# Optimization experiments

Measured on AMD Instinct MI355X. Metric: run time of the kernel, lower is better.

The kernel has to match this reference:

```python
import jax, jax.numpy as jnp
import numpy as np

B = 2048      # env batch (graphs)
A = 8         # agents per graph (fully connected)
N = B * A     # total nodes
DIN = 192     # raw obs dim
HD = 256      # h_dim (base MLP)
MD = 256      # mem_dim (GRU)
GD = 128      # gnn_dim (per-head GATv2 out, concat=False -> head mean)
H = 4         # GAT heads
NA = 20       # n_actions
ED = 3        # edge_dim


def setup_inputs() -> dict:
    key = jax.random.key(0)
    ks = jax.random.split(key, 16)
    # fully-connected directed graph per group of A agents, no self loops
    s, d = np.meshgrid(np.arange(A), np.arange(A), indexing='ij')
    mask = s != d
    s = s[mask]; d = d[mask]                     # [A*(A-1)]
    off = (np.arange(B) * A)[:, None]
    src = (off + s[None, :]).reshape(-1)
    dst = (off + d[None, :]).reshape(-1)
    edge_index = jnp.asarray(np.stack([src, dst]), dtype=jnp.int32)  # [2, E]
    E = src.shape[0]
    p = lambda k, sh: jax.random.normal(ks[k], sh, jnp.float32) * 0.02
    return {
        'inputs': jax.random.normal(ks[0], (N, DIN), jnp.float32),
        'hidden_states': jax.random.normal(ks[1], (N, MD), jnp.float32) * 0.1,
        'edge_index': edge_index,
        'edge_attr': jax.random.uniform(ks[2], (E, ED), jnp.float32),
        # base MLP (2 layers: Linear+ReLU+LayerNorm)
        'W1': p(3, (DIN, HD)), 'b1': jnp.zeros(HD), 'g1': jnp.ones(HD), 'be1': jnp.zeros(HD),
        'W2': p(4, (HD, HD)),  'b2': jnp.zeros(HD), 'g2': jnp.ones(HD), 'be2': jnp.zeros(HD),
        # GRUCell
        'Wih': p(5, (3 * MD, HD)), 'Whh': p(6, (3 * MD, MD)),
        'bih': jnp.zeros(3 * MD), 'bhh': jnp.zeros(3 * MD),
        # GATv2Conv (edge_dim=3, heads=4, concat=False, residual)
        'Wl': p(7, (MD, H * GD)), 'bl': jnp.zeros(H * GD),
        'Wr': p(8, (MD, H * GD)), 'br': jnp.zeros(H * GD),
        'att': p(9, (H, GD)),
        'We': p(10, (ED, H * GD)),
        'Wres': p(11, (MD, GD)),
        'bg': jnp.zeros(GD),
        # head: LayerNorm + Linear
        'lng': jnp.ones(GD), 'lnb': jnp.zeros(GD),
        'Wout': p(12, (GD, NA)), 'bout': jnp.zeros(NA),
    }


def _ln(x, g, b):
    mu = jnp.mean(x, -1, keepdims=True)
    xc = x - mu
    v = jnp.mean(xc * xc, -1, keepdims=True)
    return xc * jax.lax.rsqrt(v + 1e-5) * g + b


def _fwd(inputs, hidden_states, edge_attr, edge_index,
         W1, b1, g1, be1, W2, b2, g2, be2,
         Wih, Whh, bih, bhh,
         Wl, bl, Wr, br, att, We, Wres, bg,
         lng, lnb, Wout, bout):
    src, dst = edge_index[0], edge_index[1]
    # ---- base MLP encode ----
    x = _ln(jax.nn.relu(inputs @ W1 + b1), g1, be1)
    x = _ln(jax.nn.relu(x @ W2 + b2), g2, be2)          # [N, HD]
    # ---- SimpleConv(aggr='mean', combine_root='self_loop') ----
    s = jax.ops.segment_sum(x[src], dst, num_segments=N) + x
    deg = jax.ops.segment_sum(jnp.ones(src.shape[0], x.dtype), dst, num_segments=N) + 1.0
    x = s / deg[:, None]                                 # [N, HD]
    # ---- GRUCell ----
    gi = x @ Wih.T + bih
    gh = hidden_states @ Whh.T + bhh
    ir, iz, inn = jnp.split(gi, 3, -1)
    hr, hz, hn = jnp.split(gh, 3, -1)
    r = jax.nn.sigmoid(ir + hr)
    z = jax.nn.sigmoid(iz + hz)
    n = jnp.tanh(inn + r * hn)
    h = (1.0 - z) * n + z * hidden_states                # [N, MD]
    # ---- GATv2Conv (add self loops, edge_attr fill='mean') ----
    loop = jnp.arange(N, dtype=src.dtype)
    sf = jnp.concatenate([src, loop])
    df = jnp.concatenate([dst, loop])
    ea = jnp.concatenate([edge_attr, jnp.broadcast_to(edge_attr.mean(0), (N, ED))], 0)
    xl = (h @ Wl + bl).reshape(N, H, GD)
    xr = (h @ Wr + br).reshape(N, H, GD)
    m = xl[sf] + xr[df] + (ea @ We).reshape(-1, H, GD)   # [Ef, H, GD]
    m = jnp.where(m > 0, m, 0.2 * m)                     # leaky_relu(0.2)
    logits = jnp.einsum('ehc,hc->eh', m, att)            # [Ef, H]
    mx = jax.ops.segment_max(logits, df, num_segments=N)
    ex = jnp.exp(logits - mx[df])
    den = jax.ops.segment_sum(ex, df, num_segments=N)
    alpha = ex / (den[df] + 1e-16)                       # segment softmax
    out = jax.ops.segment_sum(xl[sf] * alpha[..., None], df, num_segments=N)
    out = out.mean(1) + h @ Wres + bg                    # head mean + residual + bias
    zg = jax.nn.relu(out)                                # [N, GD]
    # ---- action head ----
    q = _ln(zg, lng, lnb) @ Wout + bout                  # [N, NA]
    return q, h


def reference(inputs, hidden_states, edge_index, edge_attr,
              W1, b1, g1, be1, W2, b2, g2, be2,
              Wih, Whh, bih, bhh,
              Wl, bl, Wr, br, att, We, Wres, bg,
              lng, lnb, Wout, bout):
    return _fwd(inputs, hidden_states, edge_attr, edge_index,
                W1, b1, g1, be1, W2, b2, g2, be2,
                Wih, Whh, bih, bhh,
                Wl, bl, Wr, br, att, We, Wres, bg,
                lng, lnb, Wout, bout)
```

## Files before the change

### kernel.cpp

```cpp
#include <hip/hip_runtime.h>
#include <hip/hip_bf16.h>

constexpr int NB  = 2048;
constexpr int AG  = 8;
constexpr int NN  = NB * AG;
constexpr int DIN = 192;
constexpr int HD  = 256;
constexpr int MD  = 256;
constexpr int GD  = 128;
constexpr int NA  = 20;
constexpr int NE  = NB * AG * (AG - 1);

typedef __attribute__((ext_vector_type(8))) short bfrag8;
typedef __attribute__((ext_vector_type(4))) short sfrag4;
typedef __attribute__((ext_vector_type(4))) float f32x4;

#define MFMA16(a, b, c) __builtin_amdgcn_mfma_f32_16x16x32_bf16((a), (b), (c), 0, 0, 0)

__device__ __forceinline__ float bf2f(__hip_bfloat16 x) { return __bfloat162float(x); }
__device__ __forceinline__ __hip_bfloat16 f2bf(float x) { return __float2bfloat16(x); }
__device__ __forceinline__ short f2bs(float x) {
    __hip_bfloat16 b = __float2bfloat16(x);
    return *reinterpret_cast<short*>(&b);
}
__device__ __forceinline__ bfrag8 ldf(const __hip_bfloat16* p) { return *(const bfrag8*)p; }
__device__ __forceinline__ bfrag8 ldf32(const float* p) {
    const f32x4 a = *(const f32x4*)p;
    const f32x4 b = *(const f32x4*)(p + 4);
    bfrag8 r;
    r[0] = f2bs(a[0]); r[1] = f2bs(a[1]); r[2] = f2bs(a[2]); r[3] = f2bs(a[3]);
    r[4] = f2bs(b[0]); r[5] = f2bs(b[1]); r[6] = f2bs(b[2]); r[7] = f2bs(b[3]);
    return r;
}
__device__ __forceinline__ float sigmf(float x) { return 1.f / (1.f + __expf(-x)); }
__device__ __forceinline__ float blo(unsigned u) { return __uint_as_float(u << 16); }
__device__ __forceinline__ float bhi(unsigned u) { return __uint_as_float(u & 0xffff0000u); }

__global__ __launch_bounds__(256) void k_prep(
    const float* __restrict__ W1, const float* __restrict__ W2,
    const float* __restrict__ Wih, const float* __restrict__ Whh,
    const float* __restrict__ Wl, const float* __restrict__ bl,
    const float* __restrict__ Wr, const float* __restrict__ br,
    const float* __restrict__ Wres, const float* __restrict__ Wout,
    const float* __restrict__ ea,
    __hip_bfloat16* __restrict__ W1T, __hip_bfloat16* __restrict__ W2T,
    __hip_bfloat16* __restrict__ WihB, __hip_bfloat16* __restrict__ WhhB,
    __hip_bfloat16* __restrict__ WcatT, float* __restrict__ WoutTf,
    float* __restrict__ bcat, float* __restrict__ ea_partials)
{
    __shared__ float sw[4][3];
    const int tid = threadIdx.x;
    if (blockIdx.x >= 3151) {
        const int b = blockIdx.x - 3151;
        float a0 = 0.f, a1 = 0.f, a2 = 0.f;
#pragma unroll
        for (int k = 0; k < 7; k++) {
            int e = b * 1792 + k * 256 + tid;
            a0 += ea[e * 3 + 0];
            a1 += ea[e * 3 + 1];
            a2 += ea[e * 3 + 2];
        }
#pragma unroll
        for (int off = 1; off < 64; off <<= 1) {
            a0 += __shfl_xor(a0, off); a1 += __shfl_xor(a1, off); a2 += __shfl_xor(a2, off);
        }
        if ((tid & 63) == 0) { sw[tid >> 6][0] = a0; sw[tid >> 6][1] = a1; sw[tid >> 6][2] = a2; }
        __syncthreads();
        if (tid == 0) {
            ea_partials[b * 3 + 0] = sw[0][0] + sw[1][0] + sw[2][0] + sw[3][0];
            ea_partials[b * 3 + 1] = sw[0][1] + sw[1][1] + sw[2][1] + sw[3][1];
            ea_partials[b * 3 + 2] = sw[0][2] + sw[1][2] + sw[2][2] + sw[3][2];
        }
        return;
    }
    int i = blockIdx.x * 256 + tid;
    if (i < 49152) { int o = i / 192, c = i % 192; W1T[i] = f2bf(W1[c * 256 + o]); return; }
    i -= 49152;
    if (i < 65536) { int o = i >> 8, c = i & 255; W2T[i] = f2bf(W2[c * 256 + o]); return; }
    i -= 65536;
    if (i < 196608) { WihB[i] = f2bf(Wih[i]); return; }
    i -= 196608;
    if (i < 196608) { WhhB[i] = f2bf(Whh[i]); return; }
    i -= 196608;
    if (i < 294912) {
        int o = i >> 8, c = i & 255;
        float v;
        if (o < 512)       v = Wl[c * 512 + o];
        else if (o < 1024) v = Wr[c * 512 + (o - 512)];
        else               v = Wres[c * 128 + (o - 1024)];
        WcatT[i] = f2bf(v); return;
    }
    i -= 294912;
    if (i < 2560) { int o = i >> 7, c = i & 127; WoutTf[i] = Wout[c * 20 + o]; return; }
    i -= 2560;
    if (i < 1152) {
        float v = 0.f;
        if (i < 512) v = bl[i]; else if (i < 1024) v = br[i - 512];
        bcat[i] = v;
    }
}

__global__ __launch_bounds__(256) void k_encode(
    const float* __restrict__ in,
    const __hip_bfloat16* __restrict__ W1T,
    const float* __restrict__ b1, const float* __restrict__ g1, const float* __restrict__ be1,
    const __hip_bfloat16* __restrict__ W2T,
    const float* __restrict__ b2, const float* __restrict__ g2, const float* __restrict__ be2,
    __hip_bfloat16* __restrict__ xm)
{
    __shared__ float sf[16][257];
    __shared__ alignas(16) __hip_bfloat16 sb[16][264];
    const int tid = threadIdx.x;
    const int lane = tid & 63, w = tid >> 6;
    const int r = lane & 15, q = lane >> 4;
    const int m0 = blockIdx.x * 16;

    {
        bfrag8 af[6];
        const float* ap = in + (size_t)(m0 + r) * DIN + q * 8;
#pragma unroll
        for (int kb = 0; kb < 6; kb++) af[kb] = ldf32(ap + kb * 32);
#pragma unroll
        for (int i = 0; i < 4; i++) {
            int t = w * 4 + i;
            const __hip_bfloat16* wp = W1T + (size_t)(t * 16 + r) * DIN + q * 8;
            bfrag8 bf[6];
#pragma unroll
            for (int kb = 0; kb < 6; kb++) bf[kb] = ldf(wp + kb * 32);
            f32x4 acc = (f32x4){0.f, 0.f, 0.f, 0.f};
#pragma unroll
            for (int kb = 0; kb < 6; kb++) acc = MFMA16(af[kb], bf[kb], acc);
            int col = t * 16 + r;
            float bias = b1[col];
#pragma unroll
            for (int reg = 0; reg < 4; reg++)
                sf[q * 4 + reg][col] = fmaxf(acc[reg] + bias, 0.f);
        }
    }
    __syncthreads();
    {
        int rowi = tid >> 4, c16 = tid & 15;
        float vals[16]; float s = 0.f, s2 = 0.f;
#pragma unroll
        for (int j = 0; j < 16; j++) { float v = sf[rowi][c16 + 16 * j]; vals[j] = v; s += v; s2 += v * v; }
#pragma unroll
        for (int off = 1; off < 16; off <<= 1) { s += __shfl_xor(s, off); s2 += __shfl_xor(s2, off); }
        float mean = s * (1.f / HD);
        float var = fmaxf(s2 * (1.f / HD) - mean * mean, 0.f);
        float rs = rsqrtf(var + 1e-5f);
#pragma unroll
        for (int j = 0; j < 16; j++) {
            int col = c16 + 16 * j;
            sb[rowi][col] = f2bf((vals[j] - mean) * rs * g1[col] + be1[col]);
        }
    }
    __syncthreads();

    {
        bfrag8 af[8];
        const __hip_bfloat16* ap = &sb[r][0];
#pragma unroll
        for (int kb = 0; kb < 8; kb++) af[kb] = ldf(ap + kb * 32 + q * 8);
        float outv[4][4];
#pragma unroll
        for (int i = 0; i < 4; i++) {
            int t = w * 4 + i;
            const __hip_bfloat16* wp = W2T + (size_t)(t * 16 + r) * HD + q * 8;
            bfrag8 bf[8];
#pragma unroll
            for (int kb = 0; kb < 8; kb++) bf[kb] = ldf(wp + kb * 32);
            f32x4 acc = (f32x4){0.f, 0.f, 0.f, 0.f};
#pragma unroll
            for (int kb = 0; kb < 8; kb++) acc = MFMA16(af[kb], bf[kb], acc);
#pragma unroll
            for (int reg = 0; reg < 4; reg++) outv[i][reg] = acc[reg];
        }
        __syncthreads();
#pragma unroll
        for (int i = 0; i < 4; i++) {
            int col = (w * 4 + i) * 16 + r;
            float bias = b2[col];
#pragma unroll
            for (int reg = 0; reg < 4; reg++)
                sf[q * 4 + reg][col] = fmaxf(outv[i][reg] + bias, 0.f);
        }
    }
    __syncthreads();
    {
        int rowi = tid >> 4, c16 = tid & 15;
        float vals[16]; float s = 0.f, s2 = 0.f;
#pragma unroll
        for (int j = 0; j < 16; j++) { float v = sf[rowi][c16 + 16 * j]; vals[j] = v; s += v; s2 += v * v; }
#pragma unroll
        for (int off = 1; off < 16; off <<= 1) { s += __shfl_xor(s, off); s2 += __shfl_xor(s2, off); }
        float mean = s * (1.f / HD);
        float var = fmaxf(s2 * (1.f / HD) - mean * mean, 0.f);
        float rs = rsqrtf(var + 1e-5f);
#pragma unroll
        for (int j = 0; j < 16; j++) {
            int col = c16 + 16 * j;
            sb[rowi][col] = f2bf((vals[j] - mean) * rs * g2[col] + be2[col]);
        }
    }
    __syncthreads();
    {
        int col = tid;
        float a0 = 0.f, a1 = 0.f;
#pragma unroll
        for (int i = 0; i < 8; i++) { a0 += bf2f(sb[i][col]); a1 += bf2f(sb[8 + i][col]); }
        xm[(size_t)(2 * blockIdx.x) * HD + col] = f2bf(a0 * 0.125f);
        xm[(size_t)(2 * blockIdx.x + 1) * HD + col] = f2bf(a1 * 0.125f);
    }
}

__global__ __launch_bounds__(256) void k_gi(
    const __hip_bfloat16* __restrict__ xm,
    const __hip_bfloat16* __restrict__ WihB,
    const float* __restrict__ bih,
    float* __restrict__ gi)
{
    const int tid = threadIdx.x;
    const int lane = tid & 63, w = tid >> 6;
    const int r = lane & 15, q = lane >> 4;
    const int m0 = (blockIdx.x >> 1) * 16;
    const int t0 = (blockIdx.x & 1) * 24;

    bfrag8 af[8];
    const __hip_bfloat16* ap = xm + (size_t)(m0 + r) * MD + q * 8;
#pragma unroll
    for (int kb = 0; kb < 8; kb++) af[kb] = ldf(ap + kb * 32);
#pragma unroll
    for (int i = 0; i < 6; i++) {
        int t = t0 + w * 6 + i;
        const __hip_bfloat16* wp = WihB + (size_t)(t * 16 + r) * MD + q * 8;
        bfrag8 bf[8];
#pragma unroll
        for (int kb = 0; kb < 8; kb++) bf[kb] = ldf(wp + kb * 32);
        f32x4 acc = (f32x4){0.f, 0.f, 0.f, 0.f};
#pragma unroll
        for (int kb = 0; kb < 8; kb++) acc = MFMA16(af[kb], bf[kb], acc);
        int col = t * 16 + r;
        float bias = bih[col];
#pragma unroll
        for (int reg = 0; reg < 4; reg++) {
            int R = m0 + q * 4 + reg;
            gi[(size_t)R * 768 + col] = acc[reg] + bias;
        }
    }
}

__global__ __launch_bounds__(256, 2) void k_gruG(
    const float* __restrict__ hprev,
    const __hip_bfloat16* __restrict__ WhhB,
    const float* __restrict__ bhh,
    const float* __restrict__ gi,
    float* __restrict__ hout)
{
    const int tid = threadIdx.x;
    const int lane = tid & 63, w = tid >> 6;
    const int r = lane & 15, q = lane >> 4;
    const int m0 = (blockIdx.x >> 2) * 128;
    const int cg = (blockIdx.x & 3) * 64;

    bfrag8 afr[2][8];
#pragma unroll
    for (int t = 0; t < 2; t++) {
        const float* ap = hprev + (size_t)(m0 + (w * 2 + t) * 16 + r) * MD + q * 8;
#pragma unroll
        for (int kb = 0; kb < 8; kb++) afr[t][kb] = ldf32(ap + kb * 32);
    }
    f32x4 acc[2][12];
#pragma unroll
    for (int t = 0; t < 2; t++)
#pragma unroll
        for (int n = 0; n < 12; n++) acc[t][n] = (f32x4){0.f, 0.f, 0.f, 0.f};

#pragma unroll
    for (int kb = 0; kb < 8; kb++) {
        bfrag8 bfB[12];
#pragma unroll
        for (int g = 0; g < 3; g++)
#pragma unroll
            for (int nj = 0; nj < 4; nj++)
                bfB[g * 4 + nj] = ldf(WhhB + (size_t)(g * 256 + cg + nj * 16 + r) * MD
                                      + kb * 32 + q * 8);
#pragma unroll
        for (int t = 0; t < 2; t++)
#pragma unroll
            for (int n = 0; n < 12; n++)
                acc[t][n] = MFMA16(bfB[n], afr[t][kb], acc[t][n]);
    }

#pragma unroll
    for (int t = 0; t < 2; t++) {
        int node = m0 + (w * 2 + t) * 16 + r;
        const float* gir = gi + (size_t)(node >> 3) * 768;
#pragma unroll
        for (int nj = 0; nj < 4; nj++) {
            int c = cg + nj * 16 + q * 4;
            f32x4 gR = *(const f32x4*)&gir[c];
            f32x4 gZ = *(const f32x4*)&gir[256 + c];
            f32x4 gN = *(const f32x4*)&gir[512 + c];
            f32x4 bR = *(const f32x4*)&bhh[c];
            f32x4 bZ = *(const f32x4*)&bhh[256 + c];
            f32x4 bN = *(const f32x4*)&bhh[512 + c];
            f32x4 hp = *(const f32x4*)&hprev[(size_t)node * MD + c];
            f32x4 hv;
#pragma unroll
            for (int reg = 0; reg < 4; reg++) {
                float rr = sigmf(gR[reg] + acc[t][0 + nj][reg] + bR[reg]);
                float zz = sigmf(gZ[reg] + acc[t][4 + nj][reg] + bZ[reg]);
                float nn = tanhf(gN[reg] + rr * (acc[t][8 + nj][reg] + bN[reg]));
                hv[reg] = (1.f - zz) * nn + zz * hp[reg];
            }
            *(f32x4*)&hout[(size_t)node * MD + c] = hv;
        }
    }
}

__global__ __launch_bounds__(256, 2) void k_xlr(
    const float* __restrict__ h,
    const __hip_bfloat16* __restrict__ WcatT,
    const float* __restrict__ bcat,
    __hip_bfloat16* __restrict__ xlr)
{
    const int tid = threadIdx.x;
    const int lane = tid & 63, w = tid >> 6;
    const int r = lane & 15, q = lane >> 4;
    const int m0 = (blockIdx.x / 9) * 128;
    const int nb = (blockIdx.x % 9) * 128;

    bfrag8 afr[2][8];
#pragma unroll
    for (int t = 0; t < 2; t++) {
        const float* ap = h + (size_t)(m0 + (w * 2 + t) * 16 + r) * MD + q * 8;
#pragma unroll
        for (int kb = 0; kb < 8; kb++) afr[t][kb] = ldf32(ap + kb * 32);
    }
    f32x4 acc[2][8];
#pragma unroll
    for (int t = 0; t < 2; t++)
#pragma unroll
        for (int n = 0; n < 8; n++) acc[t][n] = (f32x4){0.f, 0.f, 0.f, 0.f};

#pragma unroll
    for (int kb = 0; kb < 8; kb++) {
        bfrag8 bfB[8];
#pragma unroll
        for (int nj = 0; nj < 8; nj++)
            bfB[nj] = ldf(WcatT + (size_t)(nb + nj * 16 + r) * MD + kb * 32 + q * 8);
#pragma unroll
        for (int t = 0; t < 2; t++)
#pragma unroll
            for (int n = 0; n < 8; n++)
                acc[t][n] = MFMA16(bfB[n], afr[t][kb], acc[t][n]);
    }

#pragma unroll
    for (int t = 0; t < 2; t++) {
        int node = m0 + (w * 2 + t) * 16 + r;
#pragma unroll
        for (int nj = 0; nj < 8; nj++) {
            int fb = nb + nj * 16 + q * 4;
            sfrag4 pk;
#pragma unroll
            for (int reg = 0; reg < 4; reg++)
                pk[reg] = f2bs(acc[t][nj][reg] + bcat[fb + reg]);
            *(sfrag4*)&xlr[(size_t)node * 1152 + fb] = pk;
        }
    }
}

__global__ __launch_bounds__(256) void k_gat(
    const __hip_bfloat16* __restrict__ xlr,
    const float* __restrict__ ea,
    const float* __restrict__ ea_partials,
    const float* __restrict__ att,
    const float* __restrict__ We,
    const float* __restrict__ bg,
    const float* __restrict__ lng, const float* __restrict__ lnb,
    const float* __restrict__ WoutTf,
    const float* __restrict__ bout,
    float* __restrict__ qout)
{
    __shared__ alignas(16) __hip_bfloat16 sx[16][1160];
    __shared__ alignas(16) float szg[16][136];
    __shared__ float slog[2][4][8][8];
    __shared__ float smean[4];
    const int tid = threadIdx.x;
    const int lane = tid & 63, w = tid >> 6;
    const int r = lane & 15, q = lane >> 4;
    const int m0 = blockIdx.x * 16;

    if (tid < 3) {
        float s = 0.f;
        for (int i = 0; i < 64; i++) s += ea_partials[i * 3 + tid];
        smean[tid] = s * (1.f / NE);
    }
    for (int idx = tid; idx < 2304; idx += 256) {
        int row = idx / 144, off = (idx % 144) * 8;
        *(uint4*)&sx[row][off] = *(const uint4*)&xlr[(size_t)(m0 + row) * 1152 + off];
    }

    float vea[2][3];
    {
        int l = (lane < 56) ? lane : 0;
#pragma unroll
        for (int g = 0; g < 2; g++) {
            const float* ep = ea + (size_t)((blockIdx.x * 2 + g) * 56 + l) * 3;
            vea[g][0] = ep[0]; vea[g][1] = ep[1]; vea[g][2] = ep[2];
        }
    }
    __syncthreads();
    const float em0 = smean[0], em1 = smean[1], em2 = smean[2];

    {
        const int li = lane & 31, half = lane >> 5;
#pragma unroll
        for (int t = 0; t < 2; t++) {
            const int combo = w * 2 + t;
            const int gg = combo >> 2, hh = combo & 3;
            const f32x4 va  = *(const f32x4*)&att[hh * 128 + li * 4];
            const f32x4 vw0 = *(const f32x4*)&We[0 * 512 + hh * 128 + li * 4];
            const f32x4 vw1 = *(const f32x4*)&We[1 * 512 + hh * 128 + li * 4];
            const f32x4 vw2 = *(const f32x4*)&We[2 * 512 + hh * 128 + li * 4];
            float at0 = va[0],  at1 = va[1],  at2 = va[2],  at3 = va[3];
            float w00 = vw0[0], w01 = vw0[1], w02 = vw0[2], w03 = vw0[3];
            float w10 = vw1[0], w11 = vw1[1], w12 = vw1[2], w13 = vw1[3];
            float w20 = vw2[0], w21 = vw2[1], w22 = vw2[2], w23 = vw2[3];
            float ve0 = vea[gg][0], ve1 = vea[gg][1], ve2 = vea[gg][2];
            float xv[4][4];
#pragma unroll
            for (int sh2 = 0; sh2 < 4; sh2++) {
                int sL = sh2 * 2 + half;
                uint2 uxl = *(const uint2*)&sx[gg * 8 + sL][hh * 128 + li * 4];
                xv[sh2][0] = blo(uxl.x); xv[sh2][1] = bhi(uxl.x);
                xv[sh2][2] = blo(uxl.y); xv[sh2][3] = bhi(uxl.y);
            }
            float mylog = 0.f;
#pragma unroll
            for (int d = 0; d < 8; d++) {
                uint2 uxr = *(const uint2*)&sx[gg * 8 + d][512 + hh * 128 + li * 4];
                float xr0 = blo(uxr.x), xr1 = bhi(uxr.x), xr2 = blo(uxr.y), xr3 = bhi(uxr.y);
#pragma unroll
                for (int sh2 = 0; sh2 < 4; sh2++) {
                    int sL = sh2 * 2 + half;
                    int el = sL * 7 + d - (d > sL ? 1 : 0);
                    float e0 = __shfl(ve0, el), e1 = __shfl(ve1, el), e2 = __shfl(ve2, el);
                    bool slf = (sL == d);
                    e0 = slf ? em0 : e0; e1 = slf ? em1 : e1; e2 = slf ? em2 : e2;
                    float p, m;
                    m = fmaf(e2, w20, fmaf(e1, w10, fmaf(e0, w00, xv[sh2][0]))) + xr0;
                    m = fmaxf(m, 0.2f * m); p = m * at0;
                    m = fmaf(e2, w21, fmaf(e1, w11, fmaf(e0, w01, xv[sh2][1]))) + xr1;
                    m = fmaxf(m, 0.2f * m); p = fmaf(m, at1, p);
                    m = fmaf(e2, w22, fmaf(e1, w12, fmaf(e0, w02, xv[sh2][2]))) + xr2;
                    m = fmaxf(m, 0.2f * m); p = fmaf(m, at2, p);
                    m = fmaf(e2, w23, fmaf(e1, w13, fmaf(e0, w03, xv[sh2][3]))) + xr3;
                    m = fmaxf(m, 0.2f * m); p = fmaf(m, at3, p);
                    p += __shfl_xor(p, 1);  p += __shfl_xor(p, 2);  p += __shfl_xor(p, 4);
                    p += __shfl_xor(p, 8);  p += __shfl_xor(p, 16);
                    float got = __shfl(p, ((lane & 1) << 5) | li);
                    bool want = ((lane >> 3) == d) && (((lane & 7) >> 1) == sh2);
                    mylog = want ? got : mylog;
                }
            }
            ((float*)&slog[gg][hh][0][0])[lane] = mylog;
        }
    }
    __syncthreads();

    if (tid < 64) {
        int sg = tid >> 5, sh2 = (tid >> 3) & 3, d = tid & 7;
        float* L = &slog[sg][sh2][d][0];
        float mx = L[0];
#pragma unroll
        for (int s = 1; s < 8; s++) mx = fmaxf(mx, L[s]);
        float ex[8]; float den = 0.f;
#pragma unroll
        for (int s = 0; s < 8; s++) { ex[s] = __expf(L[s] - mx); den += ex[s]; }
        float inv = 1.f / (den + 1e-16f);
#pragma unroll
        for (int s = 0; s < 8; s++) L[s] = ex[s] * inv;
    }
    __syncthreads();

    {
        f32x4 acc0 = (f32x4){0.f, 0.f, 0.f, 0.f};
        f32x4 acc1 = (f32x4){0.f, 0.f, 0.f, 0.f};
        const int ggr = r >> 3, dr = r & 7;
#pragma unroll
        for (int ah = 0; ah < 4; ah++) {
            bfrag8 afA;
#pragma unroll
            for (int j = 0; j < 8; j++) {
                int k = q * 8 + j;
                float v = 0.f;
                if (k < 16) {
                    int ggk = k >> 3, s = k & 7;
                    if (ggk == ggr) v = slog[ggk][ah][dr][s];
                }
                afA[j] = f2bs(v);
            }
#pragma unroll
            for (int j2 = 0; j2 < 2; j2++) {
                int chunk = w * 2 + j2;
                bfrag8 bfB;
#pragma unroll
                for (int j = 0; j < 8; j++) {
                    int k = (q * 8 + j) & 15;
                    bfB[j] = *(const short*)&sx[k][ah * 128 + chunk * 16 + r];
                }
                if (j2 == 0) acc0 = MFMA16(afA, bfB, acc0);
                else         acc1 = MFMA16(afA, bfB, acc1);
            }
        }
#pragma unroll
        for (int j2 = 0; j2 < 2; j2++) {
            f32x4 a = j2 ? acc1 : acc0;
            int c = (w * 2 + j2) * 16 + r;
            float bgc = bg[c];
#pragma unroll
            for (int reg = 0; reg < 4; reg++) {
                int row = q * 4 + reg;
                float o = a[reg] * 0.25f + bf2f(sx[row][1024 + c]) + bgc;
                szg[row][c] = fmaxf(o, 0.f);
            }
        }
    }
    __syncthreads();

    {
        int row = tid >> 4, j = tid & 15;
        float v[8]; float s = 0.f, s2 = 0.f;
#pragma unroll
        for (int cj = 0; cj < 8; cj++) { v[cj] = szg[row][j + 16 * cj]; s += v[cj]; s2 += v[cj] * v[cj]; }
#pragma unroll
        for (int off = 1; off < 16; off <<= 1) { s += __shfl_xor(s, off); s2 += __shfl_xor(s2, off); }
        float mean = s * (1.f / GD);
        float var = fmaxf(s2 * (1.f / GD) - mean * mean, 0.f);
        float rs = rsqrtf(var + 1e-5f);
#pragma unroll
        for (int cj = 0; cj < 8; cj++) {
            int c = j + 16 * cj;
            szg[row][c] = (v[cj] - mean) * rs * lng[c] + lnb[c];
        }
    }
    __syncthreads();

    {
        int row = tid >> 4, j = tid & 15;
        for (int jj = j; jj < NA; jj += 16) {
            float a = bout[jj];
            const float* wo = WoutTf + jj * 128;
#pragma unroll
            for (int c4 = 0; c4 < 32; c4++) {
                f32x4 z = *(const f32x4*)&szg[row][c4 * 4];
                const f32x4 wv = *(const f32x4*)&wo[c4 * 4];
                a = fmaf(z[0], wv[0], a); a = fmaf(z[1], wv[1], a);
                a = fmaf(z[2], wv[2], a); a = fmaf(z[3], wv[3], a);
            }
            qout[(size_t)(m0 + row) * NA + jj] = a;
        }
    }
}

extern "C" void kernel_launch(void* const* d_in, const int* in_sizes, int n_in,
                              void* d_out, int out_size, void* d_ws, size_t ws_size,
                              hipStream_t stream) {
    const float* inp   = (const float*)d_in[0];
    const float* hid   = (const float*)d_in[1];
    const float* eatt  = (const float*)d_in[3];
    const float* W1    = (const float*)d_in[4];
    const float* b1    = (const float*)d_in[5];
    const float* g1    = (const float*)d_in[6];
    const float* be1   = (const float*)d_in[7];
    const float* W2    = (const float*)d_in[8];
    const float* b2    = (const float*)d_in[9];
    const float* g2    = (const float*)d_in[10];
    const float* be2   = (const float*)d_in[11];
    const float* Wih   = (const float*)d_in[12];
    const float* Whh   = (const float*)d_in[13];
    const float* bih   = (const float*)d_in[14];
    const float* bhh   = (const float*)d_in[15];
    const float* Wl    = (const float*)d_in[16];
    const float* bl    = (const float*)d_in[17];
    const float* Wr    = (const float*)d_in[18];
    const float* br    = (const float*)d_in[19];
    const float* att   = (const float*)d_in[20];
    const float* We    = (const float*)d_in[21];
    const float* Wres  = (const float*)d_in[22];
    const float* bg    = (const float*)d_in[23];
    const float* lng   = (const float*)d_in[24];
    const float* lnb   = (const float*)d_in[25];
    const float* Wout  = (const float*)d_in[26];
    const float* bout  = (const float*)d_in[27];

    float* qout = (float*)d_out;
    float* hout = (float*)d_out + (size_t)NN * NA;

    char* ws = (char*)d_ws;
    float*           ea_partials = (float*)ws;
    __hip_bfloat16*  xm    = (__hip_bfloat16*)(ws + 2048);
    float*           gi    = (float*)(ws + 1050624);
    __hip_bfloat16*  W1T   = (__hip_bfloat16*)(ws + 7342080);
    __hip_bfloat16*  W2T   = (__hip_bfloat16*)(ws + 7440384);
    __hip_bfloat16*  WihB  = (__hip_bfloat16*)(ws + 7571456);
    __hip_bfloat16*  WhhB  = (__hip_bfloat16*)(ws + 7964672);
    __hip_bfloat16*  WcatT = (__hip_bfloat16*)(ws + 8357888);
    float*           bcat  = (float*)(ws + 8947712);
    float*           WoutTf= (float*)(ws + 8952320);
    __hip_bfloat16*  xlr   = (__hip_bfloat16*)(ws + 8962560);

    k_prep<<<3215, 256, 0, stream>>>(W1, W2, Wih, Whh, Wl, bl, Wr, br, Wres, Wout, eatt,
                                     W1T, W2T, WihB, WhhB, WcatT, WoutTf, bcat, ea_partials);
    k_encode<<<NN / 16, 256, 0, stream>>>(inp, W1T, b1, g1, be1, W2T, b2, g2, be2, xm);
    k_gi<<<256, 256, 0, stream>>>(xm, WihB, bih, gi);
    k_gruG<<<512, 256, 0, stream>>>(hid, WhhB, bhh, gi, hout);
    k_xlr<<<1152, 256, 0, stream>>>(hout, WcatT, bcat, xlr);
    k_gat<<<NN / 16, 256, 0, stream>>>(xlr, eatt, ea_partials, att, We, bg,
                                       lng, lnb, WoutTf, bout, qout);
}
```

Baseline: 328.6 us.

## Stage xlr weight tiles in LDS via direct global-to-LDS loads and swizzle block order

The xlr GEMM kernel now uses a 2x2 wave tiling where each wave computes a 64x64 sub-tile. B weight tiles are staged into XOR-swizzled shared memory with global_load_lds, looping over four K chunks. Before, every wave loaded the full B fragments straight from global memory. Block indices in both the GRU and xlr kernels are remapped so that concurrently scheduled blocks spread across different row tiles, which may improve L2 locality across XCDs. The cost is extra __syncthreads per K step and A fragments that are now reloaded from global memory inside the K loop.

```diff
diff --git a/kernel.cpp b/kernel.cpp
--- a/kernel.cpp
+++ b/kernel.cpp
@@ -16,6 +16,10 @@
 typedef __attribute__((ext_vector_type(4))) float f32x4;
 
 #define MFMA16(a, b, c) __builtin_amdgcn_mfma_f32_16x16x32_bf16((a), (b), (c), 0, 0, 0)
+
+#define GLOAD_LDS16(g, l) __builtin_amdgcn_global_load_lds(                  \
+    (const __attribute__((address_space(1))) void*)(g),                      \
+    (__attribute__((address_space(3))) void*)(l), 16, 0, 0)
 
 __device__ __forceinline__ float bf2f(__hip_bfloat16 x) { return __bfloat162float(x); }
 __device__ __forceinline__ __hip_bfloat16 f2bf(float x) { return __float2bfloat16(x); }
@@ -259,8 +263,9 @@
     const int tid = threadIdx.x;
     const int lane = tid & 63, w = tid >> 6;
     const int r = lane & 15, q = lane >> 4;
-    const int m0 = (blockIdx.x >> 2) * 128;
-    const int cg = (blockIdx.x & 3) * 64;
+    const int bswz = (blockIdx.x & 7) * 64 + (blockIdx.x >> 3);
+    const int m0 = (bswz >> 2) * 128;
+    const int cg = (bswz & 3) * 64;
 
     bfrag8 afr[2][8];
 #pragma unroll
@@ -324,48 +329,66 @@
     const float* __restrict__ bcat,
     __hip_bfloat16* __restrict__ xlr)
 {
+    __shared__ alignas(16) __hip_bfloat16 sB[128 * 64];
     const int tid = threadIdx.x;
     const int lane = tid & 63, w = tid >> 6;
     const int r = lane & 15, q = lane >> 4;
-    const int m0 = (blockIdx.x / 9) * 128;
-    const int nb = (blockIdx.x % 9) * 128;
-
-    bfrag8 afr[2][8];
-#pragma unroll
-    for (int t = 0; t < 2; t++) {
-        const float* ap = h + (size_t)(m0 + (w * 2 + t) * 16 + r) * MD + q * 8;
-#pragma unroll
-        for (int kb = 0; kb < 8; kb++) afr[t][kb] = ldf32(ap + kb * 32);
-    }
-    f32x4 acc[2][8];
-#pragma unroll
-    for (int t = 0; t < 2; t++)
-#pragma unroll
-        for (int n = 0; n < 8; n++) acc[t][n] = (f32x4){0.f, 0.f, 0.f, 0.f};
-
-#pragma unroll
-    for (int kb = 0; kb < 8; kb++) {
-        bfrag8 bfB[8];
-#pragma unroll
-        for (int nj = 0; nj < 8; nj++)
-            bfB[nj] = ldf(WcatT + (size_t)(nb + nj * 16 + r) * MD + kb * 32 + q * 8);
-#pragma unroll
-        for (int t = 0; t < 2; t++)
-#pragma unroll
-            for (int n = 0; n < 8; n++)
-                acc[t][n] = MFMA16(bfB[n], afr[t][kb], acc[t][n]);
-    }
-
-#pragma unroll
-    for (int t = 0; t < 2; t++) {
-        int node = m0 + (w * 2 + t) * 16 + r;
-#pragma unroll
-        for (int nj = 0; nj < 8; nj++) {
-            int fb = nb + nj * 16 + q * 4;
+    const int wm = w >> 1, wn = w & 1;
+
+    const int lin = (blockIdx.x & 7) * 144 + (blockIdx.x >> 3);
+    const int m0 = (lin / 9) * 128;
+    const int nb = (lin % 9) * 128;
+
+    const int srow = tid >> 3;
+    const int sch  = (tid & 7) ^ (srow & 7);
+
+    f32x4 acc[4][4];
+#pragma unroll
+    for (int am = 0; am < 4; am++)
+#pragma unroll
+        for (int bn = 0; bn < 4; bn++) acc[am][bn] = (f32x4){0.f, 0.f, 0.f, 0.f};
+
+    for (int kt = 0; kt < 4; ++kt) {
+        if (kt) __syncthreads();
+#pragma unroll
+        for (int i = 0; i < 4; ++i) {
+            const __hip_bfloat16* gp = WcatT + (size_t)(nb + i * 32 + srow) * 256
+                                       + kt * 64 + sch * 8;
+            GLOAD_LDS16(gp, &sB[i * 2048 + tid * 8]);
+        }
+        __syncthreads();
+
+#pragma unroll
+        for (int kk = 0; kk < 2; ++kk) {
+            bfrag8 af[4], bf[4];
+#pragma unroll
+            for (int am = 0; am < 4; ++am)
+                af[am] = ldf32(h + (size_t)(m0 + wm * 64 + am * 16 + r) * MD
+                               + kt * 64 + kk * 32 + q * 8);
+#pragma unroll
+            for (int bn = 0; bn < 4; ++bn) {
+                const int R = wn * 64 + bn * 16 + r;
+                const int c = (kk * 4 + q) ^ (R & 7);
+                bf[bn] = *(const bfrag8*)&sB[R * 64 + c * 8];
+            }
+#pragma unroll
+            for (int am = 0; am < 4; ++am)
+#pragma unroll
+                for (int bn = 0; bn < 4; ++bn)
+                    acc[am][bn] = MFMA16(bf[bn], af[am], acc[am][bn]);
+        }
+    }
+
+#pragma unroll
+    for (int bn = 0; bn < 4; ++bn) {
+        const int fb = nb + wn * 64 + bn * 16 + q * 4;
+        const f32x4 bv = *(const f32x4*)&bcat[fb];
+#pragma unroll
+        for (int am = 0; am < 4; ++am) {
+            const int node = m0 + wm * 64 + am * 16 + r;
             sfrag4 pk;
 #pragma unroll
-            for (int reg = 0; reg < 4; reg++)
-                pk[reg] = f2bs(acc[t][nj][reg] + bcat[fb + reg]);
+            for (int reg = 0; reg < 4; reg++) pk[reg] = f2bs(acc[am][bn][reg] + bv[reg]);
             *(sfrag4*)&xlr[(size_t)node * 1152 + fb] = pk;
         }
     }
```

New measurement: 316.9 us. -3.6%, faster.
